# Performance work log

Measured on AMD Instinct MI355X. Metric: run time of the kernel, lower is better.

Reference implementation:

```python
import jax, jax.numpy as jnp
import numpy as np

B, S, D, H = 2, 2048, 1024, 16
HD = D // H  # head dim = 64; scale uses sqrt(d_k/num_heads) = sqrt(D/H) since d_k==d_model


def setup_inputs() -> dict:
    key = jax.random.key(0)
    ks = jax.random.split(key, 12)
    s = 1.0 / np.sqrt(D)
    inp = {
        "Q": jax.random.normal(ks[0], (B, S, D), jnp.float32),
        "K": jax.random.normal(ks[1], (B, S, D), jnp.float32),
        "V": jax.random.normal(ks[2], (B, S, D), jnp.float32),
        "mask": jnp.tril(jnp.ones((S, S), jnp.int32))[None, None],  # [1,1,S,S] causal
        "Wq": jax.random.normal(ks[3], (D, D), jnp.float32) * s,
        "bq": jnp.zeros((D,), jnp.float32),
        "Wk": jax.random.normal(ks[4], (D, D), jnp.float32) * s,
        "bk": jnp.zeros((D,), jnp.float32),
        "Wv": jax.random.normal(ks[5], (D, D), jnp.float32) * s,
        "bv": jnp.zeros((D,), jnp.float32),
        "Wo": jax.random.normal(ks[6], (D, D), jnp.float32) * s,
        "bo": jnp.zeros((D,), jnp.float32),
    }
    return inp


def _split_heads(x):
    # [B,S,D] -> [B,H,S,HD]
    b, s, _ = x.shape
    return x.reshape(b, s, H, HD).transpose(0, 2, 1, 3)


def reference(Q, K, V, mask, Wq, bq, Wk, bk, Wv, bv, Wo, bo):
    q = _split_heads(Q @ Wq.T + bq)
    k = _split_heads(K @ Wk.T + bk)
    v = _split_heads(V @ Wv.T + bv)
    scale = 1.0 / jnp.sqrt(jnp.asarray(D / H, q.dtype))  # d_k/num_heads with d_k=d_model
    scores = jnp.einsum('bhqd,bhkd->bhqk', q, k) * scale
    scores = jnp.where(mask == 0, jnp.asarray(-1e9, scores.dtype), scores)
    probs = jax.nn.softmax(scores, axis=-1)
    z = jnp.einsum('bhqk,bhkd->bhqd', probs, v)  # [B,H,S,HD]
    z = z.transpose(0, 2, 1, 3).reshape(Q.shape[0], Q.shape[1], D)
    return z @ Wo.T + bo
```

## Files before the change

kernel.cpp:

```cpp
#include <hip/hip_runtime.h>
#include <hip/hip_bf16.h>

typedef unsigned short u16;
typedef unsigned int u32;
typedef __attribute__((ext_vector_type(2))) unsigned int u32x2;
typedef __attribute__((ext_vector_type(8))) short s16x8;
typedef __attribute__((ext_vector_type(4))) float f32x4;
typedef __attribute__((ext_vector_type(16))) float f32x16;

#define NB 2
#define NH 16
#define NS 2048
#define ND 1024
#define QSCALE 0.1803368801111244f

#define AS1(p) ((const __attribute__((address_space(1))) void*)(p))
#define AS3(p) ((__attribute__((address_space(3))) void*)(p))

__device__ __forceinline__ u16 f2bf(float f) {
  u32 u = __float_as_uint(f);
  u = u + 0x7FFFu + ((u >> 16) & 1u);
  return (u16)(u >> 16);
}

__device__ __forceinline__ float bf2f(u16 h) {
  return __uint_as_float(((u32)h) << 16);
}

__device__ __forceinline__ u32 pkbf(float a, float b) {
  __hip_bfloat162 h = __float22bfloat162_rn(make_float2(a, b));
  union { __hip_bfloat162 h; u32 u; } cv;
  cv.h = h;
  return cv.u;
}

__global__ __launch_bounds__(256) void cvt_kernel(
    const float* __restrict__ q, const float* __restrict__ k,
    const float* __restrict__ v, const float* __restrict__ wq,
    const float* __restrict__ wk, const float* __restrict__ wv,
    const float* __restrict__ wo, u16* __restrict__ Xbf,
    u16* __restrict__ Wbf) {
  const int s = blockIdx.z;
  const size_t M1 = (size_t)1024 * 1024;
  const float* src;
  u16* dst;
  if (s < 4)       { src = q + (size_t)s * M1;        dst = Xbf + (size_t)s * M1; }
  else if (s < 8)  { src = k + (size_t)(s - 4) * M1;  dst = Xbf + (size_t)s * M1; }
  else if (s < 12) { src = v + (size_t)(s - 8) * M1;  dst = Xbf + (size_t)s * M1; }
  else if (s == 12){ src = wq; dst = Wbf; }
  else if (s == 13){ src = wk; dst = Wbf + M1; }
  else if (s == 14){ src = wv; dst = Wbf + 2 * M1; }
  else             { src = wo; dst = Wbf + 3 * M1; }
  const int n4 = 1024 * 1024 / 4;
  for (int i = blockIdx.x * 256 + threadIdx.x; i < n4; i += gridDim.x * 256) {
    float4 a = ((const float4*)src)[i];
    uint2 p;
    p.x = (u32)f2bf(a.x) | ((u32)f2bf(a.y) << 16);
    p.y = (u32)f2bf(a.z) | ((u32)f2bf(a.w) << 16);
    ((uint2*)dst)[i] = p;
  }
}

__global__ __launch_bounds__(256) void gemm_qkv_fast(
    const u16* __restrict__ Xbf, const u16* __restrict__ Wbf,
    const float* __restrict__ bq, const float* __restrict__ bk,
    const float* __restrict__ bv, u16* __restrict__ qh, u16* __restrict__ kh,
    u16* __restrict__ vT) {
  const int id = blockIdx.x;
  const int xcd = id & 7, sl = id >> 3;
  const int grp = xcd * 12 + (sl >> 3);
  const int n0 = (sl & 7) * 128;
  const int which = grp >> 5;
  const int m0 = (grp & 31) * 128;

  const u16* A = Xbf + (size_t)which * 4096 * 1024;
  const u16* B = Wbf + (size_t)which * 1024 * 1024;
  const float* bias = (which == 0) ? bq : (which == 1) ? bk : bv;
  const int tid = threadIdx.x;
  const int w = tid >> 6, l = tid & 63, lr = l & 15, lg = l >> 4;
  const int wr = (w >> 1) * 64, wc = (w & 1) * 64;

  __shared__ u16 As[2][128 * 32];
  __shared__ u16 Bs[2][128 * 32];

  const int c0 = tid, c1 = 256 + tid;
  const int row0 = c0 >> 2, k40 = (c0 & 3) ^ (row0 & 3);
  const int row1 = c1 >> 2, k41 = (c1 & 3) ^ (row1 & 3);
  const u16* sa0 = A + (size_t)(m0 + row0) * 1024 + k40 * 8;
  const u16* sb0 = B + (size_t)(n0 + row0) * 1024 + k40 * 8;
  const u16* sa1 = A + (size_t)(m0 + row1) * 1024 + k41 * 8;
  const u16* sb1 = B + (size_t)(n0 + row1) * 1024 + k41 * 8;
  const int d0 = (w * 64) * 8, d1 = (256 + w * 64) * 8;

  const f32x4 fzero = {0.f, 0.f, 0.f, 0.f};
  f32x4 acc[4][4];
#pragma unroll
  for (int m = 0; m < 4; ++m)
#pragma unroll
    for (int n = 0; n < 4; ++n) acc[m][n] = fzero;

  __builtin_amdgcn_global_load_lds(AS1(sa0), AS3(As[0] + d0), 16, 0, 0);
  __builtin_amdgcn_global_load_lds(AS1(sb0), AS3(Bs[0] + d0), 16, 0, 0);
  __builtin_amdgcn_global_load_lds(AS1(sa1), AS3(As[0] + d1), 16, 0, 0);
  __builtin_amdgcn_global_load_lds(AS1(sb1), AS3(Bs[0] + d1), 16, 0, 0);
  __syncthreads();

  int cur = 0;
  for (int step = 0; step < 32; ++step) {
    if (step < 31) {
      const int k0 = (step + 1) * 32;
      __builtin_amdgcn_global_load_lds(AS1(sa0 + k0), AS3(As[cur ^ 1] + d0),
                                       16, 0, 0);
      __builtin_amdgcn_global_load_lds(AS1(sb0 + k0), AS3(Bs[cur ^ 1] + d0),
                                       16, 0, 0);
      __builtin_amdgcn_global_load_lds(AS1(sa1 + k0), AS3(As[cur ^ 1] + d1),
                                       16, 0, 0);
      __builtin_amdgcn_global_load_lds(AS1(sb1 + k0), AS3(Bs[cur ^ 1] + d1),
                                       16, 0, 0);
    }
    s16x8 af[4], bf[4];
#pragma unroll
    for (int m = 0; m < 4; ++m) {
      int row = wr + m * 16 + lr;
      af[m] = *(const s16x8*)(As[cur] + row * 32 + ((lg ^ (row & 3)) * 8));
    }
#pragma unroll
    for (int n = 0; n < 4; ++n) {
      int row = wc + n * 16 + lr;
      bf[n] = *(const s16x8*)(Bs[cur] + row * 32 + ((lg ^ (row & 3)) * 8));
    }
#pragma unroll
    for (int m = 0; m < 4; ++m)
#pragma unroll
      for (int n = 0; n < 4; ++n)
        acc[m][n] = __builtin_amdgcn_mfma_f32_16x16x32_bf16(af[m], bf[n],
                                                            acc[m][n], 0, 0, 0);
    __syncthreads();
    cur ^= 1;
  }

#pragma unroll
  for (int m = 0; m < 4; ++m) {
#pragma unroll
    for (int n = 0; n < 4; ++n) {
#pragma unroll
      for (int i = 0; i < 4; ++i) {
        int row = m0 + wr + m * 16 + 4 * lg + i;
        int col = n0 + wc + n * 16 + lr;
        float val = acc[m][n][i] + bias[col];
        if (which == 0) val *= QSCALE;
        int bbi = row >> 11, ss = row & 2047;
        int hhd = col >> 6, hd = col & 63;
        if (which == 0) {
          qh[(((size_t)bbi * NH + hhd) * NS + ss) * 64 + hd] = f2bf(val);
        } else if (which == 1) {
          kh[(((size_t)bbi * NH + hhd) * NS + ss) * 64 + hd] = f2bf(val);
        } else {
          vT[(((size_t)bbi * NH + hhd) * 64 + hd) * NS + ss] = f2bf(val);
        }
      }
    }
  }
}

__global__ __launch_bounds__(256) void gemm_out_fast(
    const u16* __restrict__ zin, const u16* __restrict__ Wbf,
    const float* __restrict__ bo, float* __restrict__ out) {
  const u16* B = Wbf + (size_t)3 * 1024 * 1024;
  const int id = blockIdx.x;
  const int xcd = id & 7, sl = id >> 3;
  const int grp = xcd * 4 + (sl >> 3);
  const int n0 = (sl & 7) * 128;
  const int m0 = grp * 128;
  const int tid = threadIdx.x;
  const int w = tid >> 6, l = tid & 63, lr = l & 15, lg = l >> 4;
  const int wr = (w >> 1) * 64, wc = (w & 1) * 64;

  __shared__ u16 As[2][128 * 32];
  __shared__ u16 Bs[2][128 * 32];

  const int c0 = tid, c1 = 256 + tid;
  const int row0 = c0 >> 2, k40 = (c0 & 3) ^ (row0 & 3);
  const int row1 = c1 >> 2, k41 = (c1 & 3) ^ (row1 & 3);
  const u16* sa0 = zin + (size_t)(m0 + row0) * 1024 + k40 * 8;
  const u16* sb0 = B + (size_t)(n0 + row0) * 1024 + k40 * 8;
  const u16* sa1 = zin + (size_t)(m0 + row1) * 1024 + k41 * 8;
  const u16* sb1 = B + (size_t)(n0 + row1) * 1024 + k41 * 8;
  const int d0 = (w * 64) * 8, d1 = (256 + w * 64) * 8;

  const f32x4 fzero = {0.f, 0.f, 0.f, 0.f};
  f32x4 acc[4][4];
#pragma unroll
  for (int m = 0; m < 4; ++m)
#pragma unroll
    for (int n = 0; n < 4; ++n) acc[m][n] = fzero;

  __builtin_amdgcn_global_load_lds(AS1(sa0), AS3(As[0] + d0), 16, 0, 0);
  __builtin_amdgcn_global_load_lds(AS1(sb0), AS3(Bs[0] + d0), 16, 0, 0);
  __builtin_amdgcn_global_load_lds(AS1(sa1), AS3(As[0] + d1), 16, 0, 0);
  __builtin_amdgcn_global_load_lds(AS1(sb1), AS3(Bs[0] + d1), 16, 0, 0);
  __syncthreads();

  int cur = 0;
  for (int step = 0; step < 32; ++step) {
    if (step < 31) {
      const int k0 = (step + 1) * 32;
      __builtin_amdgcn_global_load_lds(AS1(sa0 + k0), AS3(As[cur ^ 1] + d0),
                                       16, 0, 0);
      __builtin_amdgcn_global_load_lds(AS1(sb0 + k0), AS3(Bs[cur ^ 1] + d0),
                                       16, 0, 0);
      __builtin_amdgcn_global_load_lds(AS1(sa1 + k0), AS3(As[cur ^ 1] + d1),
                                       16, 0, 0);
      __builtin_amdgcn_global_load_lds(AS1(sb1 + k0), AS3(Bs[cur ^ 1] + d1),
                                       16, 0, 0);
    }
    s16x8 af[4], bf[4];
#pragma unroll
    for (int m = 0; m < 4; ++m) {
      int row = wr + m * 16 + lr;
      af[m] = *(const s16x8*)(As[cur] + row * 32 + ((lg ^ (row & 3)) * 8));
    }
#pragma unroll
    for (int n = 0; n < 4; ++n) {
      int row = wc + n * 16 + lr;
      bf[n] = *(const s16x8*)(Bs[cur] + row * 32 + ((lg ^ (row & 3)) * 8));
    }
#pragma unroll
    for (int m = 0; m < 4; ++m)
#pragma unroll
      for (int n = 0; n < 4; ++n)
        acc[m][n] = __builtin_amdgcn_mfma_f32_16x16x32_bf16(af[m], bf[n],
                                                            acc[m][n], 0, 0, 0);
    __syncthreads();
    cur ^= 1;
  }

#pragma unroll
  for (int m = 0; m < 4; ++m)
#pragma unroll
    for (int n = 0; n < 4; ++n)
#pragma unroll
      for (int i = 0; i < 4; ++i) {
        int row = m0 + wr + m * 16 + 4 * lg + i;
        int col = n0 + wc + n * 16 + lr;
        out[(size_t)row * 1024 + col] = acc[m][n][i] + bo[col];
      }
}

__device__ __forceinline__ void stage64(const u16* __restrict__ kh,
                                        const u16* __restrict__ vT, int bh,
                                        int t, int tid, int w, u16* kbase,
                                        u16* vbase) {
#pragma unroll
  for (int i = 0; i < 2; ++i) {
    int c = i * 256 + tid;
    int row = c >> 3, k8 = (c & 7) ^ (row & 7);
    const u16* sk = kh + ((size_t)bh * NS + t * 64 + row) * 64 + k8 * 8;
    const u16* sv = vT + ((size_t)bh * 64 + row) * NS + t * 64 + k8 * 8;
    u16* dk = kbase + (i * 256 + w * 64) * 8;
    u16* dv = vbase + (i * 256 + w * 64) * 8;
    __builtin_amdgcn_global_load_lds(AS1(sk), AS3(dk), 16, 0, 0);
    __builtin_amdgcn_global_load_lds(AS1(sv), AS3(dv), 16, 0, 0);
  }
}

__global__ __launch_bounds__(256) void attn_split_kernel(
    const u16* __restrict__ qh, const u16* __restrict__ kh,
    const u16* __restrict__ vT, u16* __restrict__ Opart,
    float* __restrict__ Mpart, float* __restrict__ Lpart) {
  const int f = blockIdx.x;
  const int bh = f & 31;
  const int pp = f >> 5;
  const int tid = threadIdx.x;
  const int w = tid >> 6, l = tid & 63;
  const int ql = l & 31, hi = l >> 5, hi8 = hi * 8;

  __shared__ u16 smem[2][2][64][64];

#pragma unroll 1
  for (int c = 0; c < 2; ++c) {
    const int band = c ? (15 - pp) : pp;
    const int t0 = c ? (16 - pp) : 0;
    const int t1 = c ? (32 - 2 * pp) : (pp + 1);
    const int q0w = band * 128 + w * 32;

    s16x8 qf[4];
    {
      const u16* qp = qh + ((size_t)bh * NS + q0w + ql) * 64 + hi8;
#pragma unroll
      for (int st = 0; st < 4; ++st) qf[st] = *(const s16x8*)(qp + st * 16);
    }

    f32x16 o0 = {0, 0, 0, 0, 0, 0, 0, 0, 0, 0, 0, 0, 0, 0, 0, 0};
    f32x16 o1 = {0, 0, 0, 0, 0, 0, 0, 0, 0, 0, 0, 0, 0, 0, 0, 0};
    float m_run = -1e30f, l_run = 0.f;

    __syncthreads();
    stage64(kh, vT, bh, t0, tid, w, &smem[t0 & 1][0][0][0],
            &smem[t0 & 1][1][0][0]);
    __syncthreads();

    for (int t = t0; t < t1; ++t) {
      if (t + 1 < t1)
        stage64(kh, vT, bh, t + 1, tid, w, &smem[(t + 1) & 1][0][0][0],
                &smem[(t + 1) & 1][1][0][0]);
      const u16* kp = &smem[t & 1][0][0][0];
      const u16* vp = &smem[t & 1][1][0][0];

      const int kvg0 = t * 64, kvg1 = t * 64 + 32;
      if (kvg0 <= q0w) {
        f32x16 s0 = {0, 0, 0, 0, 0, 0, 0, 0, 0, 0, 0, 0, 0, 0, 0, 0};
        f32x16 s1 = {0, 0, 0, 0, 0, 0, 0, 0, 0, 0, 0, 0, 0, 0, 0, 0};
        const int kr0 = ql, kr1 = 32 + ql;
        __builtin_amdgcn_s_setprio(1);
#pragma unroll
        for (int st = 0; st < 4; ++st) {
          s16x8 ak = *(const s16x8*)(kp + kr0 * 64 +
                                     (((st * 2 + hi) ^ (kr0 & 7)) * 8));
          s0 = __builtin_amdgcn_mfma_f32_32x32x16_bf16(ak, qf[st], s0, 0, 0, 0);
        }
        if (kvg1 <= q0w) {
#pragma unroll
          for (int st = 0; st < 4; ++st) {
            s16x8 ak = *(const s16x8*)(kp + kr1 * 64 +
                                       (((st * 2 + hi) ^ (kr1 & 7)) * 8));
            s1 = __builtin_amdgcn_mfma_f32_32x32x16_bf16(ak, qf[st], s1, 0, 0,
                                                         0);
          }
        }
        __builtin_amdgcn_s_setprio(0);

        if (kvg0 == q0w) {
#pragma unroll
          for (int r = 0; r < 16; ++r) {
            int kvloc = (r & 3) + 8 * (r >> 2) + 4 * hi;
            if (kvloc > ql) s0[r] = -1e30f;
          }
        }
        if (kvg1 > q0w) {
#pragma unroll
          for (int r = 0; r < 16; ++r) s1[r] = -1e30f;
        } else if (kvg1 == q0w) {
#pragma unroll
          for (int r = 0; r < 16; ++r) {
            int kvloc = (r & 3) + 8 * (r >> 2) + 4 * hi;
            if (kvloc > ql) s1[r] = -1e30f;
          }
        }

        float mr[16];
#pragma unroll
        for (int r = 0; r < 16; ++r) mr[r] = fmaxf(s0[r], s1[r]);
#pragma unroll
        for (int off = 8; off; off >>= 1)
#pragma unroll
          for (int r = 0; r < 8; ++r)
            if (r < off) mr[r] = fmaxf(mr[r], mr[r + off]);
        float mx = mr[0];
        {
          u32x2 rm = __builtin_amdgcn_permlane32_swap(
              __float_as_uint(mx), __float_as_uint(mx), 0, 0);
          mx = fmaxf(__uint_as_float(rm.x), __uint_as_float(rm.y));
        }

        if (!__all(mx - m_run <= 8.0f)) {
          float mnew = fmaxf(m_run, mx);
          float fs = __builtin_amdgcn_exp2f(m_run - mnew);
#pragma unroll
          for (int r = 0; r < 16; ++r) {
            o0[r] *= fs;
            o1[r] *= fs;
          }
          l_run *= fs;
          m_run = mnew;
        }

        float ps = 0.f;
        u32 pk0[8], pk1[8];
#pragma unroll
        for (int tt = 0; tt < 8; ++tt) {
          float a = __builtin_amdgcn_exp2f(s0[2 * tt] - m_run);
          float b = __builtin_amdgcn_exp2f(s0[2 * tt + 1] - m_run);
          ps += a + b;
          pk0[tt] = pkbf(a, b);
        }
#pragma unroll
        for (int tt = 0; tt < 8; ++tt) {
          float a = __builtin_amdgcn_exp2f(s1[2 * tt] - m_run);
          float b = __builtin_amdgcn_exp2f(s1[2 * tt + 1] - m_run);
          ps += a + b;
          pk1[tt] = pkbf(a, b);
        }
        {
          u32x2 rp = __builtin_amdgcn_permlane32_swap(
              __float_as_uint(ps), __float_as_uint(ps), 0, 0);
          ps = __uint_as_float(rp.x) + __uint_as_float(rp.y);
        }
        l_run += ps;

        u32x2 e0 = __builtin_amdgcn_permlane32_swap(pk0[0], pk0[2], 0, 0);
        u32x2 e1 = __builtin_amdgcn_permlane32_swap(pk0[1], pk0[3], 0, 0);
        u32x2 e2 = __builtin_amdgcn_permlane32_swap(pk0[4], pk0[6], 0, 0);
        u32x2 e3 = __builtin_amdgcn_permlane32_swap(pk0[5], pk0[7], 0, 0);
        u32x2 e4 = __builtin_amdgcn_permlane32_swap(pk1[0], pk1[2], 0, 0);
        u32x2 e5 = __builtin_amdgcn_permlane32_swap(pk1[1], pk1[3], 0, 0);
        u32x2 e6 = __builtin_amdgcn_permlane32_swap(pk1[4], pk1[6], 0, 0);
        u32x2 e7 = __builtin_amdgcn_permlane32_swap(pk1[5], pk1[7], 0, 0);
        union { u32 u[4]; s16x8 h; } pf[4];
        pf[0].u[0] = e0.x; pf[0].u[1] = e1.x; pf[0].u[2] = e0.y; pf[0].u[3] = e1.y;
        pf[1].u[0] = e2.x; pf[1].u[1] = e3.x; pf[1].u[2] = e2.y; pf[1].u[3] = e3.y;
        pf[2].u[0] = e4.x; pf[2].u[1] = e5.x; pf[2].u[2] = e4.y; pf[2].u[3] = e5.y;
        pf[3].u[0] = e6.x; pf[3].u[1] = e7.x; pf[3].u[2] = e6.y; pf[3].u[3] = e7.y;

        __builtin_amdgcn_s_setprio(1);
#pragma unroll
        for (int ks = 0; ks < 4; ++ks) {
          int ch = ks * 2 + hi;
          s16x8 av0 = *(const s16x8*)(vp + ql * 64 + ((ch ^ (ql & 7)) * 8));
          s16x8 av1 =
              *(const s16x8*)(vp + (32 + ql) * 64 + ((ch ^ (ql & 7)) * 8));
          o0 = __builtin_amdgcn_mfma_f32_32x32x16_bf16(av0, pf[ks].h, o0, 0, 0,
                                                       0);
          o1 = __builtin_amdgcn_mfma_f32_32x32x16_bf16(av1, pf[ks].h, o1, 0, 0,
                                                       0);
        }
        __builtin_amdgcn_s_setprio(0);
      }
      __syncthreads();
    }

    u16* Zw = &smem[0][0][0][0] + w * (32 * 72);
#pragma unroll
    for (int r = 0; r < 16; r += 2) {
      int d0 = (r & 3) + 8 * (r >> 2) + 4 * hi;
      *(u32*)&Zw[ql * 72 + d0]      = pkbf(o0[r], o0[r + 1]);
      *(u32*)&Zw[ql * 72 + 32 + d0] = pkbf(o1[r], o1[r + 1]);
    }
    if (hi == 0) {
      size_t mix = ((size_t)c * 32 + bh) * NS + q0w + ql;
      Mpart[mix] = m_run;
      Lpart[mix] = l_run;
    }
#pragma unroll
    for (int i = 0; i < 4; ++i) {
      int cid = i * 64 + l;
      int row = cid >> 3, c8 = (cid & 7) * 8;
      s16x8 vv = *(const s16x8*)&Zw[row * 72 + c8];
      *(s16x8*)(Opart + (((size_t)c * 32 + bh) * NS + q0w + row) * 64 + c8) =
          vv;
    }
  }
}

__global__ __launch_bounds__(256) void attn_combine_kernel(
    const u16* __restrict__ Opart, const float* __restrict__ Mpart,
    const float* __restrict__ Lpart, u16* __restrict__ z) {
  const int tok = blockIdx.x;
  const int bb = tok >> 11, ss = tok & 2047;
  const int t = threadIdx.x;
  const int d4 = t * 4;
  const int hh = d4 >> 6;
  const size_t qix = ((size_t)bb * NH + hh) * NS + ss;
  const size_t stride = (size_t)32 * NS;

  float m0 = Mpart[qix], l0 = Lpart[qix];
  float m1 = Mpart[qix + stride], l1 = Lpart[qix + stride];
  float mm = fmaxf(m0, m1);
  float w0 = __builtin_amdgcn_exp2f(m0 - mm);
  float w1 = __builtin_amdgcn_exp2f(m1 - mm);
  float inv = 1.f / (w0 * l0 + w1 * l1);
  w0 *= inv;
  w1 *= inv;

  size_t ob = qix * 64 + (d4 & 63);
  uint2 a = *(const uint2*)(Opart + ob);
  uint2 b = *(const uint2*)(Opart + ob + stride * 64);

  float z0 = bf2f((u16)(a.x & 0xffff)) * w0 + bf2f((u16)(b.x & 0xffff)) * w1;
  float z1 = bf2f((u16)(a.x >> 16)) * w0 + bf2f((u16)(b.x >> 16)) * w1;
  float z2 = bf2f((u16)(a.y & 0xffff)) * w0 + bf2f((u16)(b.y & 0xffff)) * w1;
  float z3 = bf2f((u16)(a.y >> 16)) * w0 + bf2f((u16)(b.y >> 16)) * w1;

  uint2 p;
  p.x = pkbf(z0, z1);
  p.y = pkbf(z2, z3);
  *(uint2*)(z + ((size_t)bb * NS + ss) * ND + d4) = p;
}

__global__ __launch_bounds__(128) void attn_kernel(
    const u16* __restrict__ qh, const u16* __restrict__ kh,
    const u16* __restrict__ vT, u16* __restrict__ z) {
  const int f = blockIdx.x;
  const int bh = f & 31;
  const int j0 = (f >> 5) & 7;
  const int g = f >> 8;
  const int mb = 2 * j0;
  const int m =
      (g == 0) ? mb : (g == 1) ? mb + 1 : (g == 2) ? 30 - mb : 31 - mb;
  const int bb = bh >> 4, hh = bh & 15;
  const int tid = threadIdx.x;
  const int w = tid >> 6, l = tid & 63;
  const int ql = l & 31, hi = l >> 5, hi8 = hi * 8;
  const int q0w = m * 64 + w * 32;

  __shared__ u16 smem[2][2][64][64];

  s16x8 qf[4];
  {
    const u16* qp = qh + ((size_t)bh * NS + q0w + ql) * 64 + hi8;
#pragma unroll
    for (int st = 0; st < 4; ++st) qf[st] = *(const s16x8*)(qp + st * 16);
  }

  f32x16 o0 = {0, 0, 0, 0, 0, 0, 0, 0, 0, 0, 0, 0, 0, 0, 0, 0};
  f32x16 o1 = {0, 0, 0, 0, 0, 0, 0, 0, 0, 0, 0, 0, 0, 0, 0, 0};
  float m_run = -1e30f, l_run = 0.f;

  const int ntiles = m + 1;

#pragma unroll
  for (int i = 0; i < 4; ++i) {
    int c = i * 128 + tid;
    int row = c >> 3, k8 = (c & 7) ^ (row & 7);
    const u16* sk = kh + ((size_t)bh * NS + row) * 64 + k8 * 8;
    const u16* sv = vT + ((size_t)bh * 64 + row) * NS + k8 * 8;
    u16* dk = &smem[0][0][0][0] + (i * 128 + w * 64) * 8;
    u16* dv = &smem[0][1][0][0] + (i * 128 + w * 64) * 8;
    __builtin_amdgcn_global_load_lds(AS1(sk), AS3(dk), 16, 0, 0);
    __builtin_amdgcn_global_load_lds(AS1(sv), AS3(dv), 16, 0, 0);
  }
  __syncthreads();

  for (int t = 0; t < ntiles; ++t) {
    if (t + 1 < ntiles) {
      int b1 = (t + 1) & 1;
#pragma unroll
      for (int i = 0; i < 4; ++i) {
        int c = i * 128 + tid;
        int row = c >> 3, k8 = (c & 7) ^ (row & 7);
        const u16* sk =
            kh + ((size_t)bh * NS + (t + 1) * 64 + row) * 64 + k8 * 8;
        const u16* sv =
            vT + ((size_t)bh * 64 + row) * NS + (t + 1) * 64 + k8 * 8;
        u16* dk = &smem[b1][0][0][0] + (i * 128 + w * 64) * 8;
        u16* dv = &smem[b1][1][0][0] + (i * 128 + w * 64) * 8;
        __builtin_amdgcn_global_load_lds(AS1(sk), AS3(dk), 16, 0, 0);
        __builtin_amdgcn_global_load_lds(AS1(sv), AS3(dv), 16, 0, 0);
      }
    }
    const u16* kp = &smem[t & 1][0][0][0];
    const u16* vp = &smem[t & 1][1][0][0];

#pragma unroll
    for (int sub = 0; sub < 2; ++sub) {
      const int kvg = t * 64 + sub * 32;
      if (kvg > q0w) continue;
      const bool masked = (kvg == q0w);

      const int kr = sub * 32 + ql;
      f32x16 s = {0, 0, 0, 0, 0, 0, 0, 0, 0, 0, 0, 0, 0, 0, 0, 0};
#pragma unroll
      for (int st = 0; st < 4; ++st) {
        s16x8 ak = *(const s16x8*)(kp + kr * 64 +
                                   (((st * 2 + hi) ^ (kr & 7)) * 8));
        s = __builtin_amdgcn_mfma_f32_32x32x16_bf16(ak, qf[st], s, 0, 0, 0);
      }

      float sv_[16];
#pragma unroll
      for (int r = 0; r < 16; ++r) {
        float x = s[r];
        if (masked) {
          int kvloc = (r & 3) + 8 * (r >> 2) + 4 * hi;
          if (kvloc > ql) x = -1e30f;
        }
        sv_[r] = x;
      }

      float mx = sv_[0];
#pragma unroll
      for (int r = 1; r < 16; ++r) mx = fmaxf(mx, sv_[r]);
      {
        u32x2 rm = __builtin_amdgcn_permlane32_swap(__float_as_uint(mx),
                                                    __float_as_uint(mx), 0, 0);
        mx = fmaxf(__uint_as_float(rm.x), __uint_as_float(rm.y));
      }

      if (__any(mx > m_run)) {
        float mnew = fmaxf(m_run, mx);
        float fs = __builtin_amdgcn_exp2f(m_run - mnew);
#pragma unroll
        for (int r = 0; r < 16; ++r) {
          o0[r] *= fs;
          o1[r] *= fs;
        }
        l_run *= fs;
        m_run = mnew;
      }

      float ps = 0.f;
      u32 pk[8];
#pragma unroll
      for (int tt = 0; tt < 8; ++tt) {
        float a = __builtin_amdgcn_exp2f(sv_[2 * tt] - m_run);
        float b = __builtin_amdgcn_exp2f(sv_[2 * tt + 1] - m_run);
        ps += a + b;
        pk[tt] = pkbf(a, b);
      }
      {
        u32x2 rp = __builtin_amdgcn_permlane32_swap(__float_as_uint(ps),
                                                    __float_as_uint(ps), 0, 0);
        ps = __uint_as_float(rp.x) + __uint_as_float(rp.y);
      }
      l_run += ps;

      u32x2 e0 = __builtin_amdgcn_permlane32_swap(pk[0], pk[2], 0, 0);
      u32x2 e1 = __builtin_amdgcn_permlane32_swap(pk[1], pk[3], 0, 0);
      u32x2 e2 = __builtin_amdgcn_permlane32_swap(pk[4], pk[6], 0, 0);
      u32x2 e3 = __builtin_amdgcn_permlane32_swap(pk[5], pk[7], 0, 0);
      union { u32 u[4]; s16x8 h; } pf0, pf1;
      pf0.u[0] = e0.x; pf0.u[1] = e1.x; pf0.u[2] = e0.y; pf0.u[3] = e1.y;
      pf1.u[0] = e2.x; pf1.u[1] = e3.x; pf1.u[2] = e2.y; pf1.u[3] = e3.y;

#pragma unroll
      for (int k2 = 0; k2 < 2; ++k2) {
        s16x8 pa = (k2 == 0) ? pf0.h : pf1.h;
        int ch = sub * 4 + k2 * 2 + hi;
        s16x8 av0 = *(const s16x8*)(vp + ql * 64 + ((ch ^ (ql & 7)) * 8));
        s16x8 av1 =
            *(const s16x8*)(vp + (32 + ql) * 64 + ((ch ^ (ql & 7)) * 8));
        o0 = __builtin_amdgcn_mfma_f32_32x32x16_bf16(av0, pa, o0, 0, 0, 0);
        o1 = __builtin_amdgcn_mfma_f32_32x32x16_bf16(av1, pa, o1, 0, 0, 0);
      }
    }
    __syncthreads();
  }

  float inv = 1.f / l_run;
  u16* Zw = &smem[0][0][0][0] + w * (32 * 72);
#pragma unroll
  for (int r = 0; r < 16; r += 2) {
    int d0 = (r & 3) + 8 * (r >> 2) + 4 * hi;
    *(u32*)&Zw[ql * 72 + d0]      = pkbf(o0[r] * inv, o0[r + 1] * inv);
    *(u32*)&Zw[ql * 72 + 32 + d0] = pkbf(o1[r] * inv, o1[r + 1] * inv);
  }
#pragma unroll
  for (int i = 0; i < 4; ++i) {
    int cid = i * 64 + l;
    int row = cid >> 3, c8 = (cid & 7) * 8;
    s16x8 vv = *(const s16x8*)&Zw[row * 72 + c8];
    *(s16x8*)(z + ((size_t)bb * NS + q0w + row) * ND + hh * 64 + c8) = vv;
  }
}

__global__ __launch_bounds__(256) void proj_qkv_kernel(
    const float* __restrict__ Qin, const float* __restrict__ Kin,
    const float* __restrict__ Vin,
    const float* __restrict__ Wq, const float* __restrict__ bq,
    const float* __restrict__ Wk, const float* __restrict__ bk,
    const float* __restrict__ Wv, const float* __restrict__ bv,
    u16* __restrict__ qh, u16* __restrict__ kh, u16* __restrict__ vT) {
  const int which = blockIdx.z;
  const float* X = (which == 0) ? Qin : (which == 1) ? Kin : Vin;
  const float* W = (which == 0) ? Wq : (which == 1) ? Wk : Wv;
  const float* bias = (which == 0) ? bq : (which == 1) ? bk : bv;

  const int m0 = blockIdx.y * 128, n0 = blockIdx.x * 128;
  const int tid = threadIdx.x;
  const int w = tid >> 6, l = tid & 63, lr = l & 15, lg = l >> 4;
  const int wr = (w >> 1) * 64, wc = (w & 1) * 64;

  __shared__ u16 As[128][40];
  __shared__ u16 Bs[128][40];

  const f32x4 fzero = {0.f, 0.f, 0.f, 0.f};
  f32x4 acc[4][4];
#pragma unroll
  for (int m = 0; m < 4; ++m)
#pragma unroll
    for (int n = 0; n < 4; ++n) acc[m][n] = fzero;

  for (int k0 = 0; k0 < 1024; k0 += 32) {
#pragma unroll
    for (int i = 0; i < 4; ++i) {
      int idx = tid + i * 256;
      int row = idx >> 3, c4 = (idx & 7) * 4;
      float4 a = *(const float4*)(X + (size_t)(m0 + row) * 1024 + k0 + c4);
      *(u32*)&As[row][c4]     = (u32)f2bf(a.x) | ((u32)f2bf(a.y) << 16);
      *(u32*)&As[row][c4 + 2] = (u32)f2bf(a.z) | ((u32)f2bf(a.w) << 16);
      float4 b = *(const float4*)(W + (size_t)(n0 + row) * 1024 + k0 + c4);
      *(u32*)&Bs[row][c4]     = (u32)f2bf(b.x) | ((u32)f2bf(b.y) << 16);
      *(u32*)&Bs[row][c4 + 2] = (u32)f2bf(b.z) | ((u32)f2bf(b.w) << 16);
    }
    __syncthreads();
    s16x8 af[4], bf[4];
#pragma unroll
    for (int m = 0; m < 4; ++m)
      af[m] = *(const s16x8*)&As[wr + m * 16 + lr][lg * 8];
#pragma unroll
    for (int n = 0; n < 4; ++n)
      bf[n] = *(const s16x8*)&Bs[wc + n * 16 + lr][lg * 8];
#pragma unroll
    for (int m = 0; m < 4; ++m)
#pragma unroll
      for (int n = 0; n < 4; ++n)
        acc[m][n] = __builtin_amdgcn_mfma_f32_16x16x32_bf16(af[m], bf[n],
                                                            acc[m][n], 0, 0, 0);
    __syncthreads();
  }

  u16* dst01 = (which == 0) ? qh : kh;
#pragma unroll
  for (int m = 0; m < 4; ++m) {
#pragma unroll
    for (int n = 0; n < 4; ++n) {
#pragma unroll
      for (int i = 0; i < 4; ++i) {
        int row = m0 + wr + m * 16 + 4 * lg + i;
        int col = n0 + wc + n * 16 + lr;
        float val = acc[m][n][i] + bias[col];
        if (which == 0) val *= QSCALE;
        int bbi = row >> 11, ss = row & 2047;
        int hhd = col >> 6, hd = col & 63;
        if (which < 2) {
          dst01[(((size_t)bbi * NH + hhd) * NS + ss) * 64 + hd] = f2bf(val);
        } else {
          vT[(((size_t)bbi * NH + hhd) * 64 + hd) * NS + ss] = f2bf(val);
        }
      }
    }
  }
}

__global__ __launch_bounds__(256) void proj_out_kernel(
    const u16* __restrict__ zin, const float* __restrict__ Wo,
    const float* __restrict__ bo, float* __restrict__ out) {
  const int m0 = blockIdx.y * 128, n0 = blockIdx.x * 128;
  const int tid = threadIdx.x;
  const int w = tid >> 6, l = tid & 63, lr = l & 15, lg = l >> 4;
  const int wr = (w >> 1) * 64, wc = (w & 1) * 64;

  __shared__ u16 As[128][40];
  __shared__ u16 Bs[128][40];

  const f32x4 fzero = {0.f, 0.f, 0.f, 0.f};
  f32x4 acc[4][4];
#pragma unroll
  for (int m = 0; m < 4; ++m)
#pragma unroll
    for (int n = 0; n < 4; ++n) acc[m][n] = fzero;

  for (int k0 = 0; k0 < 1024; k0 += 32) {
#pragma unroll
    for (int i = 0; i < 2; ++i) {
      int idx = tid + i * 256;
      int row = idx >> 2, c8 = (idx & 3) * 8;
      *(s16x8*)&As[row][c8] =
          *(const s16x8*)(zin + (size_t)(m0 + row) * 1024 + k0 + c8);
    }
#pragma unroll
    for (int i = 0; i < 4; ++i) {
      int idx = tid + i * 256;
      int row = idx >> 3, c4 = (idx & 7) * 4;
      float4 b = *(const float4*)(Wo + (size_t)(n0 + row) * 1024 + k0 + c4);
      *(u32*)&Bs[row][c4]     = (u32)f2bf(b.x) | ((u32)f2bf(b.y) << 16);
      *(u32*)&Bs[row][c4 + 2] = (u32)f2bf(b.z) | ((u32)f2bf(b.w) << 16);
    }
    __syncthreads();
    s16x8 af[4], bf[4];
#pragma unroll
    for (int m = 0; m < 4; ++m)
      af[m] = *(const s16x8*)&As[wr + m * 16 + lr][lg * 8];
#pragma unroll
    for (int n = 0; n < 4; ++n)
      bf[n] = *(const s16x8*)&Bs[wc + n * 16 + lr][lg * 8];
#pragma unroll
    for (int m = 0; m < 4; ++m)
#pragma unroll
      for (int n = 0; n < 4; ++n)
        acc[m][n] = __builtin_amdgcn_mfma_f32_16x16x32_bf16(af[m], bf[n],
                                                            acc[m][n], 0, 0, 0);
    __syncthreads();
  }

#pragma unroll
  for (int m = 0; m < 4; ++m)
#pragma unroll
    for (int n = 0; n < 4; ++n)
#pragma unroll
      for (int i = 0; i < 4; ++i) {
        int row = m0 + wr + m * 16 + 4 * lg + i;
        int col = n0 + wc + n * 16 + lr;
        out[(size_t)row * 1024 + col] = acc[m][n][i] + bo[col];
      }
}

extern "C" void kernel_launch(void* const* d_in, const int* in_sizes, int n_in,
                              void* d_out, int out_size, void* d_ws,
                              size_t ws_size, hipStream_t stream) {
  const float* Q = (const float*)d_in[0];
  const float* K = (const float*)d_in[1];
  const float* V = (const float*)d_in[2];
  const float* Wq = (const float*)d_in[4];
  const float* bq = (const float*)d_in[5];
  const float* Wk = (const float*)d_in[6];
  const float* bk = (const float*)d_in[7];
  const float* Wv = (const float*)d_in[8];
  const float* bv = (const float*)d_in[9];
  const float* Wo = (const float*)d_in[10];
  const float* bo = (const float*)d_in[11];
  float* out = (float*)d_out;

  const size_t M1 = (size_t)1024 * 1024;
  u16* base = (u16*)d_ws;

  if (ws_size >= (size_t)58720256) {
    u16* Wbf = base;
    u16* qh = base + 4 * M1;
    u16* zz = qh;
    u16* kh = base + 8 * M1;
    u16* vT = base + 12 * M1;
    u16* Xbf = base + 16 * M1;
    u16* Opart = base + 16 * M1;
    float* Mpart = (float*)(base + 24 * M1);
    float* Lpart = (float*)(base + 24 * M1 + 256 * 1024);

    cvt_kernel<<<dim3(128, 1, 16), 256, 0, stream>>>(Q, K, V, Wq, Wk, Wv, Wo,
                                                     Xbf, Wbf);
    gemm_qkv_fast<<<dim3(768), 256, 0, stream>>>(Xbf, Wbf, bq, bk, bv, qh, kh,
                                                 vT);
    attn_split_kernel<<<dim3(512), 256, 0, stream>>>(qh, kh, vT, Opart, Mpart,
                                                     Lpart);
    attn_combine_kernel<<<dim3(4096), 256, 0, stream>>>(Opart, Mpart, Lpart,
                                                        zz);
    gemm_out_fast<<<dim3(256), 256, 0, stream>>>(zz, Wbf, bo, out);
  } else {
    u16* qh = base;
    u16* kh = base + 4 * M1;
    u16* vT = base + 8 * M1;
    u16* zz = base + 12 * M1;
    proj_qkv_kernel<<<dim3(8, 32, 3), 256, 0, stream>>>(Q, K, V, Wq, bq, Wk,
                                                        bk, Wv, bv, qh, kh, vT);
    attn_kernel<<<dim3(1024), 128, 0, stream>>>(qh, kh, vT, zz);
    proj_out_kernel<<<dim3(8, 32), 256, 0, stream>>>(zz, Wo, bo, out);
  }
}
```

Baseline: 148.6 us.

## Prefetch two K-tiles ahead in GEMMs with explicit waitcnt barriers and plain grid mapping

```diff
diff --git a/kernel.cpp b/kernel.cpp
--- a/kernel.cpp
+++ b/kernel.cpp
@@ -66,13 +66,8 @@
     const float* __restrict__ bq, const float* __restrict__ bk,
     const float* __restrict__ bv, u16* __restrict__ qh, u16* __restrict__ kh,
     u16* __restrict__ vT) {
-  const int id = blockIdx.x;
-  const int xcd = id & 7, sl = id >> 3;
-  const int grp = xcd * 12 + (sl >> 3);
-  const int n0 = (sl & 7) * 128;
-  const int which = grp >> 5;
-  const int m0 = (grp & 31) * 128;
-
+  const int which = blockIdx.z;
+  const int m0 = blockIdx.y * 128, n0 = blockIdx.x * 128;
   const u16* A = Xbf + (size_t)which * 4096 * 1024;
   const u16* B = Wbf + (size_t)which * 1024 * 1024;
   const float* bias = (which == 0) ? bq : (which == 1) ? bk : bv;
@@ -99,25 +94,21 @@
 #pragma unroll
     for (int n = 0; n < 4; ++n) acc[m][n] = fzero;
 
-  __builtin_amdgcn_global_load_lds(AS1(sa0), AS3(As[0] + d0), 16, 0, 0);
-  __builtin_amdgcn_global_load_lds(AS1(sb0), AS3(Bs[0] + d0), 16, 0, 0);
-  __builtin_amdgcn_global_load_lds(AS1(sa1), AS3(As[0] + d1), 16, 0, 0);
-  __builtin_amdgcn_global_load_lds(AS1(sb1), AS3(Bs[0] + d1), 16, 0, 0);
-  __syncthreads();
+  auto STAGE = [&](int buf, int k0) {
+    __builtin_amdgcn_global_load_lds(AS1(sa0 + k0), AS3(As[buf] + d0), 16, 0, 0);
+    __builtin_amdgcn_global_load_lds(AS1(sb0 + k0), AS3(Bs[buf] + d0), 16, 0, 0);
+    __builtin_amdgcn_global_load_lds(AS1(sa1 + k0), AS3(As[buf] + d1), 16, 0, 0);
+    __builtin_amdgcn_global_load_lds(AS1(sb1 + k0), AS3(Bs[buf] + d1), 16, 0, 0);
+  };
+
+  STAGE(0, 0);
+  STAGE(1, 32);
+  asm volatile("s_waitcnt vmcnt(4)" ::: "memory");
+  __builtin_amdgcn_sched_barrier(0);
+  __builtin_amdgcn_s_barrier();
 
   int cur = 0;
   for (int step = 0; step < 32; ++step) {
-    if (step < 31) {
-      const int k0 = (step + 1) * 32;
-      __builtin_amdgcn_global_load_lds(AS1(sa0 + k0), AS3(As[cur ^ 1] + d0),
-                                       16, 0, 0);
-      __builtin_amdgcn_global_load_lds(AS1(sb0 + k0), AS3(Bs[cur ^ 1] + d0),
-                                       16, 0, 0);
-      __builtin_amdgcn_global_load_lds(AS1(sa1 + k0), AS3(As[cur ^ 1] + d1),
-                                       16, 0, 0);
-      __builtin_amdgcn_global_load_lds(AS1(sb1 + k0), AS3(Bs[cur ^ 1] + d1),
-                                       16, 0, 0);
-    }
     s16x8 af[4], bf[4];
 #pragma unroll
     for (int m = 0; m < 4; ++m) {
@@ -129,13 +120,28 @@
       int row = wc + n * 16 + lr;
       bf[n] = *(const s16x8*)(Bs[cur] + row * 32 + ((lg ^ (row & 3)) * 8));
     }
+    asm volatile("s_waitcnt lgkmcnt(0)" ::: "memory");
+    __builtin_amdgcn_sched_barrier(0);
+    __builtin_amdgcn_s_barrier();
+
+    const bool stg = (step + 2 < 32);
+    if (stg) STAGE(cur, (step + 2) * 32);
+
+    __builtin_amdgcn_s_setprio(1);
 #pragma unroll
     for (int m = 0; m < 4; ++m)
 #pragma unroll
       for (int n = 0; n < 4; ++n)
         acc[m][n] = __builtin_amdgcn_mfma_f32_16x16x32_bf16(af[m], bf[n],
                                                             acc[m][n], 0, 0, 0);
-    __syncthreads();
+    __builtin_amdgcn_s_setprio(0);
+
+    if (stg)
+      asm volatile("s_waitcnt vmcnt(4)" ::: "memory");
+    else
+      asm volatile("s_waitcnt vmcnt(0)" ::: "memory");
+    __builtin_amdgcn_sched_barrier(0);
+    __builtin_amdgcn_s_barrier();
     cur ^= 1;
   }
 
@@ -167,11 +173,7 @@
     const u16* __restrict__ zin, const u16* __restrict__ Wbf,
     const float* __restrict__ bo, float* __restrict__ out) {
   const u16* B = Wbf + (size_t)3 * 1024 * 1024;
-  const int id = blockIdx.x;
-  const int xcd = id & 7, sl = id >> 3;
-  const int grp = xcd * 4 + (sl >> 3);
-  const int n0 = (sl & 7) * 128;
-  const int m0 = grp * 128;
+  const int m0 = blockIdx.y * 128, n0 = blockIdx.x * 128;
   const int tid = threadIdx.x;
   const int w = tid >> 6, l = tid & 63, lr = l & 15, lg = l >> 4;
   const int wr = (w >> 1) * 64, wc = (w & 1) * 64;
@@ -195,25 +197,21 @@
 #pragma unroll
     for (int n = 0; n < 4; ++n) acc[m][n] = fzero;
 
-  __builtin_amdgcn_global_load_lds(AS1(sa0), AS3(As[0] + d0), 16, 0, 0);
-  __builtin_amdgcn_global_load_lds(AS1(sb0), AS3(Bs[0] + d0), 16, 0, 0);
-  __builtin_amdgcn_global_load_lds(AS1(sa1), AS3(As[0] + d1), 16, 0, 0);
-  __builtin_amdgcn_global_load_lds(AS1(sb1), AS3(Bs[0] + d1), 16, 0, 0);
-  __syncthreads();
+  auto STAGE = [&](int buf, int k0) {
+    __builtin_amdgcn_global_load_lds(AS1(sa0 + k0), AS3(As[buf] + d0), 16, 0, 0);
+    __builtin_amdgcn_global_load_lds(AS1(sb0 + k0), AS3(Bs[buf] + d0), 16, 0, 0);
+    __builtin_amdgcn_global_load_lds(AS1(sa1 + k0), AS3(As[buf] + d1), 16, 0, 0);
+    __builtin_amdgcn_global_load_lds(AS1(sb1 + k0), AS3(Bs[buf] + d1), 16, 0, 0);
+  };
+
+  STAGE(0, 0);
+  STAGE(1, 32);
+  asm volatile("s_waitcnt vmcnt(4)" ::: "memory");
+  __builtin_amdgcn_sched_barrier(0);
+  __builtin_amdgcn_s_barrier();
 
   int cur = 0;
   for (int step = 0; step < 32; ++step) {
-    if (step < 31) {
-      const int k0 = (step + 1) * 32;
-      __builtin_amdgcn_global_load_lds(AS1(sa0 + k0), AS3(As[cur ^ 1] + d0),
-                                       16, 0, 0);
-      __builtin_amdgcn_global_load_lds(AS1(sb0 + k0), AS3(Bs[cur ^ 1] + d0),
-                                       16, 0, 0);
-      __builtin_amdgcn_global_load_lds(AS1(sa1 + k0), AS3(As[cur ^ 1] + d1),
-                                       16, 0, 0);
-      __builtin_amdgcn_global_load_lds(AS1(sb1 + k0), AS3(Bs[cur ^ 1] + d1),
-                                       16, 0, 0);
-    }
     s16x8 af[4], bf[4];
 #pragma unroll
     for (int m = 0; m < 4; ++m) {
@@ -225,13 +223,28 @@
       int row = wc + n * 16 + lr;
       bf[n] = *(const s16x8*)(Bs[cur] + row * 32 + ((lg ^ (row & 3)) * 8));
     }
+    asm volatile("s_waitcnt lgkmcnt(0)" ::: "memory");
+    __builtin_amdgcn_sched_barrier(0);
+    __builtin_amdgcn_s_barrier();
+
+    const bool stg = (step + 2 < 32);
+    if (stg) STAGE(cur, (step + 2) * 32);
+
+    __builtin_amdgcn_s_setprio(1);
 #pragma unroll
     for (int m = 0; m < 4; ++m)
 #pragma unroll
       for (int n = 0; n < 4; ++n)
         acc[m][n] = __builtin_amdgcn_mfma_f32_16x16x32_bf16(af[m], bf[n],
                                                             acc[m][n], 0, 0, 0);
-    __syncthreads();
+    __builtin_amdgcn_s_setprio(0);
+
+    if (stg)
+      asm volatile("s_waitcnt vmcnt(4)" ::: "memory");
+    else
+      asm volatile("s_waitcnt vmcnt(0)" ::: "memory");
+    __builtin_amdgcn_sched_barrier(0);
+    __builtin_amdgcn_s_barrier();
     cur ^= 1;
   }
 
@@ -827,13 +840,13 @@
 
     cvt_kernel<<<dim3(128, 1, 16), 256, 0, stream>>>(Q, K, V, Wq, Wk, Wv, Wo,
                                                      Xbf, Wbf);
-    gemm_qkv_fast<<<dim3(768), 256, 0, stream>>>(Xbf, Wbf, bq, bk, bv, qh, kh,
-                                                 vT);
+    gemm_qkv_fast<<<dim3(8, 32, 3), 256, 0, stream>>>(Xbf, Wbf, bq, bk, bv,
+                                                      qh, kh, vT);
     attn_split_kernel<<<dim3(512), 256, 0, stream>>>(qh, kh, vT, Opart, Mpart,
                                                      Lpart);
     attn_combine_kernel<<<dim3(4096), 256, 0, stream>>>(Opart, Mpart, Lpart,
                                                         zz);
-    gemm_out_fast<<<dim3(256), 256, 0, stream>>>(zz, Wbf, bo, out);
+    gemm_out_fast<<<dim3(8, 32), 256, 0, stream>>>(zz, Wbf, bo, out);
   } else {
     u16* qh = base;
     u16* kh = base + 4 * M1;
```

Measured after the change: 132.6 us. -10.8%, faster.
